# Kernel tuning notes

Hardware: AMD Instinct MI355X
Metric: run time of the kernel (lower is better)

The kernel has to match this reference:

```python
import jax, jax.numpy as jnp
import numpy as np

DIM = 512
NUM_HEADS = 8
HEAD_DIM = DIM // NUM_HEADS


def setup_inputs() -> dict:
    key = jax.random.key(0)
    ks = jax.random.split(key, 9)
    s = 1.0 / np.sqrt(DIM)
    x = jax.random.normal(ks[0], (2, 4096, DIM), dtype=jnp.float32)
    Wq = jax.random.uniform(ks[1], (DIM, DIM), jnp.float32, -s, s)
    bq = jax.random.uniform(ks[2], (DIM,), jnp.float32, -s, s)
    Wk = jax.random.uniform(ks[3], (DIM, DIM), jnp.float32, -s, s)
    bk = jax.random.uniform(ks[4], (DIM,), jnp.float32, -s, s)
    Wv = jax.random.uniform(ks[5], (DIM, DIM), jnp.float32, -s, s)
    bv = jax.random.uniform(ks[6], (DIM,), jnp.float32, -s, s)
    Wo = jax.random.uniform(ks[7], (DIM, DIM), jnp.float32, -s, s)
    bo = jax.random.uniform(ks[8], (DIM,), jnp.float32, -s, s)
    return {"x": x, "Wq": Wq, "bq": bq, "Wk": Wk, "bk": bk,
            "Wv": Wv, "bv": bv, "Wo": Wo, "bo": bo}


def reference(x, Wq, bq, Wk, bk, Wv, bv, Wo, bo):
    B, S, D = x.shape
    H, Hd = NUM_HEADS, HEAD_DIM
    # Linear layers (torch stores weight as [out,in]; here W is [in,out])
    q = (x @ Wq + bq).reshape(B, S, H, Hd).transpose(0, 2, 1, 3)  # [B,H,S,Hd]
    k = (x @ Wk + bk).reshape(B, S, H, Hd).transpose(0, 2, 1, 3)
    v = (x @ Wv + bv).reshape(B, S, H, Hd).transpose(0, 2, 1, 3)
    # NOTE: original scales by dim**0.5, not head_dim**0.5
    energy = jnp.einsum('bhqd,bhkd->bhqk', q, k) / jnp.sqrt(jnp.float32(D))
    attn = jax.nn.softmax(energy, axis=-1)
    out = jnp.einsum('bhqk,bhkd->bhqd', attn, v)
    out = out.transpose(0, 2, 1, 3).reshape(B, S, D)
    return out @ Wo + bo
```

## Files before the change

kernel.cpp:

```cpp
#include <hip/hip_runtime.h>

typedef unsigned short USH;
typedef short s16x8 __attribute__((ext_vector_type(8)));
typedef float f32x4 __attribute__((ext_vector_type(4)));
typedef float f32x4v __attribute__((ext_vector_type(4)));
typedef unsigned int u32x4 __attribute__((ext_vector_type(4)));
typedef s16x8 s16x8_a __attribute__((may_alias));
typedef f32x4v f32x4v_a __attribute__((may_alias));
typedef u32x4 u32x4_a __attribute__((may_alias));
typedef unsigned long long u64_a __attribute__((may_alias));

#if __has_builtin(__builtin_amdgcn_exp2f)
#define EXP2F(x) __builtin_amdgcn_exp2f(x)
#else
#define EXP2F(x) __builtin_exp2f(x)
#endif

__device__ __forceinline__ USH f2bf(float f) {
  union { float f; unsigned int i; } c; c.f = f;
  unsigned int x = c.i;
  return (USH)((x + 0x7FFFu + ((x >> 16) & 1u)) >> 16);
}
__device__ __forceinline__ unsigned int pk_bf16(float a, float b) {
  union { float f; unsigned int i; } ca, cb; ca.f = a; cb.f = b;
  return ((ca.i + 0x8000u) >> 16) | ((cb.i + 0x8000u) & 0xFFFF0000u);
}

__device__ __forceinline__ f32x4 mfma16(s16x8 a, s16x8 b, f32x4 c) {
  return __builtin_amdgcn_mfma_f32_16x16x32_bf16(a, b, c, 0, 0, 0);
}

__global__ void transpose_w(const float* __restrict__ Wq, const float* __restrict__ Wk,
                            const float* __restrict__ Wv, const float* __restrict__ Wo,
                            USH* __restrict__ wsT) {
  __shared__ float tile[32][33];
  const int z = blockIdx.z;
  const float* W = (z == 0) ? Wq : (z == 1) ? Wk : (z == 2) ? Wv : Wo;
  USH* WT = wsT + (size_t)z * 262144;
  const int n0 = blockIdx.x * 32, k0 = blockIdx.y * 32;
  const int tx = threadIdx.x, ty = threadIdx.y;
  #pragma unroll
  for (int i = 0; i < 4; ++i)
    tile[ty + i * 8][tx] = W[(size_t)(k0 + ty + i * 8) * 512 + n0 + tx];
  __syncthreads();
  #pragma unroll
  for (int i = 0; i < 4; ++i)
    WT[(size_t)(n0 + ty + i * 8) * 512 + k0 + tx] = f2bf(tile[tx][ty + i * 8]);
}

__global__ __launch_bounds__(256) void cvt_x(const float* __restrict__ x,
                                             USH* __restrict__ xb) {
  const size_t i = ((size_t)blockIdx.x * 256 + threadIdx.x) * 8;
  const f32x4v a = *(const f32x4v_a*)(x + i);
  const f32x4v b = *(const f32x4v_a*)(x + i + 4);
  u32x4 s;
  s.x = pk_bf16(a.x, a.y); s.y = pk_bf16(a.z, a.w);
  s.z = pk_bf16(b.x, b.y); s.w = pk_bf16(b.z, b.w);
  *(u32x4_a*)(xb + i) = s;
}

template <int MODE>
__global__ __launch_bounds__(256, 2) void gemm_bias(
    const USH* __restrict__ A, const USH* __restrict__ BT0,
    const float* __restrict__ b0, const float* __restrict__ b1,
    const float* __restrict__ b2,
    USH* __restrict__ oQ, USH* __restrict__ oKV, float* __restrict__ oF) {
  __shared__ __align__(16) USH As[128 * 36];
  __shared__ __align__(16) USH Bs[128 * 36];
  const int z = blockIdx.z;
  const USH* BT = BT0 + (size_t)z * 262144;
  const float* bias = (z == 0) ? b0 : ((z == 1) ? b1 : b2);
  USH* outb = (z == 0) ? oQ : (oKV + (size_t)(z - 1) * 4194304);
  const float qs = (MODE == 1 && z == 0) ? 0.06375871528132839f : 1.0f;

  const int t = threadIdx.x;
  const int w = t >> 6, lane = t & 63;
  const int c = lane & 15, g = lane >> 4;
  const int wm = w & 1, wn = w >> 1;
  const int m0 = blockIdx.x * 128, n0 = blockIdx.y * 128;
  const int srow = t >> 1, scol = (t & 1) * 16;

  f32x4 acc[4][4] = {};

  const USH* Ap0 = A + (size_t)(m0 + srow) * 512 + scol;
  const USH* Bp0 = BT + (size_t)(n0 + srow) * 512 + scol;
  s16x8 pa0 = *(const s16x8_a*)(Ap0);
  s16x8 pa1 = *(const s16x8_a*)(Ap0 + 8);
  s16x8 pb0 = *(const s16x8_a*)(Bp0);
  s16x8 pb1 = *(const s16x8_a*)(Bp0 + 8);

  for (int kt = 0; kt < 16; ++kt) {
    __syncthreads();
    *(s16x8_a*)(As + srow * 36 + scol) = pa0;
    *(s16x8_a*)(As + srow * 36 + scol + 8) = pa1;
    *(s16x8_a*)(Bs + srow * 36 + scol) = pb0;
    *(s16x8_a*)(Bs + srow * 36 + scol + 8) = pb1;
    const int ktn = (kt < 15) ? kt + 1 : kt;
    pa0 = *(const s16x8_a*)(Ap0 + ktn * 32);
    pa1 = *(const s16x8_a*)(Ap0 + ktn * 32 + 8);
    pb0 = *(const s16x8_a*)(Bp0 + ktn * 32);
    pb1 = *(const s16x8_a*)(Bp0 + ktn * 32 + 8);
    __syncthreads();
    s16x8 af[4], bfr[4];
    #pragma unroll
    for (int i = 0; i < 4; ++i) {
      af[i]  = *(const s16x8_a*)(As + (wm * 64 + i * 16 + c) * 36 + g * 8);
      bfr[i] = *(const s16x8_a*)(Bs + (wn * 64 + i * 16 + c) * 36 + g * 8);
    }
    #pragma unroll
    for (int mf = 0; mf < 4; ++mf)
      #pragma unroll
      for (int nf = 0; nf < 4; ++nf)
        acc[mf][nf] = mfma16(af[mf], bfr[nf], acc[mf][nf]);
  }

  #pragma unroll
  for (int nf = 0; nf < 4; ++nf) {
    const int n = n0 + wn * 64 + nf * 16 + c;
    const float bv = bias[n];
    #pragma unroll
    for (int mf = 0; mf < 4; ++mf)
      #pragma unroll
      for (int r = 0; r < 4; ++r) {
        const int m = m0 + wm * 64 + mf * 16 + g * 4 + r;
        const float v = (acc[mf][nf][r] + bv) * qs;
        if (MODE == 0) {
          oF[(size_t)m * 512 + n] = v;
        } else {
          const int bb = m >> 12, s = m & 4095, h = n >> 6, hd = n & 63;
          if (z == 2)
            outb[(((size_t)(bb * 8 + h)) * 64 + hd) * 4096 + s] = f2bf(v);
          else
            outb[(((size_t)(bb * 8 + h)) * 4096 + s) * 64 + hd] = f2bf(v);
        }
      }
  }
}

__global__ __launch_bounds__(256, 2) void attn(const USH* __restrict__ Qbuf,
                                               const USH* __restrict__ kv,
                                               USH* __restrict__ att) {
  __shared__ __align__(16) USH Ks[2 * 64 * 36];
  __shared__ __align__(16) USH Vt[64 * 76];
  __shared__ __align__(16) USH Ps[4][32 * 76];
  __shared__ float lbuf[4][32];

  const int t = threadIdx.x;
  const int w = t >> 6, lane = t & 63;
  const int c = lane & 15, g = lane >> 4;
  const int bh = blockIdx.y;
  const int bb = bh >> 3, hh = bh & 7;
  const size_t base = (size_t)bh * 262144;
  const USH* Q = Qbuf + base;
  const USH* K = kv + base;
  const USH* V = kv + 4194304 + base;
  const int q0 = blockIdx.x * 128 + w * 32;

  s16x8 qf[2][2];
  #pragma unroll
  for (int colf = 0; colf < 2; ++colf)
    #pragma unroll
    for (int kh = 0; kh < 2; ++kh)
      qf[colf][kh] = *(const s16x8_a*)(Q + (size_t)(q0 + colf * 16 + c) * 64 + kh * 32 + g * 8);

  s16x8 onesf;
  {
    const short one = (short)0x3F80, val = (c == 0) ? one : (short)0;
    #pragma unroll
    for (int j = 0; j < 8; ++j) onesf[j] = val;
  }

  f32x4 o[2][4] = {};
  f32x4 o_l[2] = {};
  const int kr = t >> 2, kc = (t & 3) * 16;
  const USH* Kp0 = K + (size_t)kr * 64 + kc;
  const USH* Vp0 = V + (size_t)kr * 4096 + kc;
  const int khalf = kc >> 5, koff = kc & 31;

  s16x8 pk0 = *(const s16x8_a*)(Kp0);
  s16x8 pk1 = *(const s16x8_a*)(Kp0 + 8);
  s16x8 pv0 = *(const s16x8_a*)(Vp0);
  s16x8 pv1 = *(const s16x8_a*)(Vp0 + 8);

  for (int kt = 0; kt < 64; ++kt) {
    __syncthreads();
    *(s16x8_a*)(Ks + khalf * 2304 + kr * 36 + koff) = pk0;
    *(s16x8_a*)(Ks + khalf * 2304 + kr * 36 + koff + 8) = pk1;
    *(s16x8_a*)(Vt + kr * 76 + kc) = pv0;
    *(s16x8_a*)(Vt + kr * 76 + kc + 8) = pv1;
    const int ktn = (kt < 63) ? kt + 1 : kt;
    pk0 = *(const s16x8_a*)(Kp0 + (size_t)ktn * 4096);
    pk1 = *(const s16x8_a*)(Kp0 + (size_t)ktn * 4096 + 8);
    pv0 = *(const s16x8_a*)(Vp0 + ktn * 64);
    pv1 = *(const s16x8_a*)(Vp0 + ktn * 64 + 8);
    __syncthreads();

    f32x4 st[4][2] = {};
    #pragma unroll
    for (int kh = 0; kh < 2; ++kh) {
      s16x8 ak[4];
      #pragma unroll
      for (int kff = 0; kff < 4; ++kff)
        ak[kff] = *(const s16x8_a*)(Ks + kh * 2304 + (kff * 16 + c) * 36 + g * 8);
      #pragma unroll
      for (int kff = 0; kff < 4; ++kff)
        #pragma unroll
        for (int colf = 0; colf < 2; ++colf)
          st[kff][colf] = mfma16(ak[kff], qf[colf][kh], st[kff][colf]);
    }

    #pragma unroll
    for (int colf = 0; colf < 2; ++colf)
      #pragma unroll
      for (int kff = 0; kff < 4; ++kff)
        #pragma unroll
        for (int r = 0; r < 4; ++r)
          st[kff][colf][r] = EXP2F(st[kff][colf][r]);

    #pragma unroll
    for (int colf = 0; colf < 2; ++colf)
      #pragma unroll
      for (int kff = 0; kff < 4; ++kff) {
        const unsigned int lo = pk_bf16(st[kff][colf][0], st[kff][colf][1]);
        const unsigned int hi = pk_bf16(st[kff][colf][2], st[kff][colf][3]);
        const unsigned long long pk64 =
            (unsigned long long)lo | ((unsigned long long)hi << 32);
        *(u64_a*)(&Ps[w][(c + 16 * colf) * 76 + kff * 16 + g * 4]) = pk64;
      }

    #pragma unroll
    for (int kf = 0; kf < 2; ++kf) {
      s16x8 ap[2], bv[4];
      #pragma unroll
      for (int mf = 0; mf < 2; ++mf)
        ap[mf] = *(const s16x8_a*)(&Ps[w][(mf * 16 + c) * 76 + kf * 32 + g * 8]);
      #pragma unroll
      for (int hf = 0; hf < 4; ++hf)
        bv[hf] = *(const s16x8_a*)(&Vt[(c + 16 * hf) * 76 + kf * 32 + g * 8]);
      #pragma unroll
      for (int mf = 0; mf < 2; ++mf) {
        #pragma unroll
        for (int hf = 0; hf < 4; ++hf)
          o[mf][hf] = mfma16(ap[mf], bv[hf], o[mf][hf]);
        o_l[mf] = mfma16(ap[mf], onesf, o_l[mf]);
      }
    }
  }

  if (c == 0) {
    #pragma unroll
    for (int mf = 0; mf < 2; ++mf)
      #pragma unroll
      for (int r = 0; r < 4; ++r)
        lbuf[w][mf * 16 + g * 4 + r] = o_l[mf][r];
  }
  __syncthreads();

  #pragma unroll
  for (int mf = 0; mf < 2; ++mf)
    #pragma unroll
    for (int r = 0; r < 4; ++r) {
      const int ml = mf * 16 + g * 4 + r;
      const float linv = 1.0f / lbuf[w][ml];
      const int qrow = q0 + ml;
      #pragma unroll
      for (int hf = 0; hf < 4; ++hf) {
        const int hd = c + 16 * hf;
        att[((size_t)(bb * 4096 + qrow)) * 512 + hh * 64 + hd] =
            f2bf(o[mf][hf][r] * linv);
      }
    }
}

extern "C" void kernel_launch(void* const* d_in, const int* in_sizes, int n_in,
                              void* d_out, int out_size, void* d_ws, size_t ws_size,
                              hipStream_t stream) {
  (void)in_sizes; (void)n_in; (void)out_size; (void)ws_size;
  const float* x  = (const float*)d_in[0];
  const float* Wq = (const float*)d_in[1];
  const float* bq = (const float*)d_in[2];
  const float* Wk = (const float*)d_in[3];
  const float* bk = (const float*)d_in[4];
  const float* Wv = (const float*)d_in[5];
  const float* bv = (const float*)d_in[6];
  const float* Wo = (const float*)d_in[7];
  const float* bo = (const float*)d_in[8];
  USH* ws  = (USH*)d_ws;
  USH* wT  = ws;
  USH* kv  = ws + 1048576;
  USH* att = ws + 1048576 + 8388608;
  float* outF = (float*)d_out;
  USH* qscratch = (USH*)d_out;
  USH* xb = (USH*)d_out + 4194304;

  transpose_w<<<dim3(16, 16, 4), dim3(32, 8), 0, stream>>>(Wq, Wk, Wv, Wo, wT);
  cvt_x<<<2048, 256, 0, stream>>>(x, xb);
  gemm_bias<1><<<dim3(64, 4, 3), 256, 0, stream>>>(xb, wT, bq, bk, bv,
                                                   qscratch, kv, nullptr);
  attn<<<dim3(32, 16), 256, 0, stream>>>(qscratch, kv, att);
  gemm_bias<0><<<dim3(64, 4, 1), 256, 0, stream>>>(att, wT + 3 * 262144, bo, bo, bo,
                                                   nullptr, nullptr, outF);
}
```

Before: 215.1 us.

## Double-buffer LDS tiles, fuse prep kernels, use hardware bf16 pack

Double-buffers the shared-memory K/V and GEMM tiles so each loop iteration needs only one barrier instead of two. Merges the weight transpose and x conversion into a single prep launch. Uses the native packed bf16 conversion builtin when the compiler provides it, and raises the GEMM occupancy hint to 3. This doubles LDS use for those tiles, and the rounding of the builtin may differ slightly from the manual rounding it replaces.

After: 225.1 us. 4.7% more time.

```diff
diff --git a/kernel.cpp b/kernel.cpp
--- a/kernel.cpp
+++ b/kernel.cpp
@@ -22,23 +22,46 @@
   return (USH)((x + 0x7FFFu + ((x >> 16) & 1u)) >> 16);
 }
 __device__ __forceinline__ unsigned int pk_bf16(float a, float b) {
+#if __has_builtin(__builtin_amdgcn_cvt_pk_bf16_f32)
+  typedef USH ush2 __attribute__((ext_vector_type(2)));
+  union { ush2 v; unsigned int u; } r;
+  r.v = __builtin_amdgcn_cvt_pk_bf16_f32(a, b);
+  return r.u;
+#else
   union { float f; unsigned int i; } ca, cb; ca.f = a; cb.f = b;
   return ((ca.i + 0x8000u) >> 16) | ((cb.i + 0x8000u) & 0xFFFF0000u);
+#endif
 }
 
 __device__ __forceinline__ f32x4 mfma16(s16x8 a, s16x8 b, f32x4 c) {
   return __builtin_amdgcn_mfma_f32_16x16x32_bf16(a, b, c, 0, 0, 0);
 }
 
-__global__ void transpose_w(const float* __restrict__ Wq, const float* __restrict__ Wk,
-                            const float* __restrict__ Wv, const float* __restrict__ Wo,
-                            USH* __restrict__ wsT) {
+__global__ __launch_bounds__(256) void prep(
+    const float* __restrict__ Wq, const float* __restrict__ Wk,
+    const float* __restrict__ Wv, const float* __restrict__ Wo,
+    const float* __restrict__ x, USH* __restrict__ wsT, USH* __restrict__ xb) {
   __shared__ float tile[32][33];
   const int z = blockIdx.z;
+  const int t = threadIdx.x;
+  if (z == 4) {
+    const size_t b0 = ((size_t)blockIdx.y * 16 + blockIdx.x) * 16384;
+    #pragma unroll
+    for (int j = 0; j < 8; ++j) {
+      const size_t i = b0 + (size_t)j * 2048 + t * 8;
+      const f32x4v a = *(const f32x4v_a*)(x + i);
+      const f32x4v b = *(const f32x4v_a*)(x + i + 4);
+      u32x4 s;
+      s.x = pk_bf16(a.x, a.y); s.y = pk_bf16(a.z, a.w);
+      s.z = pk_bf16(b.x, b.y); s.w = pk_bf16(b.z, b.w);
+      *(u32x4_a*)(xb + i) = s;
+    }
+    return;
+  }
   const float* W = (z == 0) ? Wq : (z == 1) ? Wk : (z == 2) ? Wv : Wo;
   USH* WT = wsT + (size_t)z * 262144;
   const int n0 = blockIdx.x * 32, k0 = blockIdx.y * 32;
-  const int tx = threadIdx.x, ty = threadIdx.y;
+  const int tx = t & 31, ty = t >> 5;
   #pragma unroll
   for (int i = 0; i < 4; ++i)
     tile[ty + i * 8][tx] = W[(size_t)(k0 + ty + i * 8) * 512 + n0 + tx];
@@ -48,25 +71,14 @@
     WT[(size_t)(n0 + ty + i * 8) * 512 + k0 + tx] = f2bf(tile[tx][ty + i * 8]);
 }
 
-__global__ __launch_bounds__(256) void cvt_x(const float* __restrict__ x,
-                                             USH* __restrict__ xb) {
-  const size_t i = ((size_t)blockIdx.x * 256 + threadIdx.x) * 8;
-  const f32x4v a = *(const f32x4v_a*)(x + i);
-  const f32x4v b = *(const f32x4v_a*)(x + i + 4);
-  u32x4 s;
-  s.x = pk_bf16(a.x, a.y); s.y = pk_bf16(a.z, a.w);
-  s.z = pk_bf16(b.x, b.y); s.w = pk_bf16(b.z, b.w);
-  *(u32x4_a*)(xb + i) = s;
-}
-
 template <int MODE>
-__global__ __launch_bounds__(256, 2) void gemm_bias(
+__global__ __launch_bounds__(256, 3) void gemm_bias(
     const USH* __restrict__ A, const USH* __restrict__ BT0,
     const float* __restrict__ b0, const float* __restrict__ b1,
     const float* __restrict__ b2,
     USH* __restrict__ oQ, USH* __restrict__ oKV, float* __restrict__ oF) {
-  __shared__ __align__(16) USH As[128 * 36];
-  __shared__ __align__(16) USH Bs[128 * 36];
+  __shared__ __align__(16) USH As[2][128 * 36];
+  __shared__ __align__(16) USH Bs[2][128 * 36];
   const int z = blockIdx.z;
   const USH* BT = BT0 + (size_t)z * 262144;
   const float* bias = (z == 0) ? b0 : ((z == 1) ? b1 : b2);
@@ -90,22 +102,22 @@
   s16x8 pb1 = *(const s16x8_a*)(Bp0 + 8);
 
   for (int kt = 0; kt < 16; ++kt) {
+    const int buf = kt & 1;
+    *(s16x8_a*)(As[buf] + srow * 36 + scol) = pa0;
+    *(s16x8_a*)(As[buf] + srow * 36 + scol + 8) = pa1;
+    *(s16x8_a*)(Bs[buf] + srow * 36 + scol) = pb0;
+    *(s16x8_a*)(Bs[buf] + srow * 36 + scol + 8) = pb1;
     __syncthreads();
-    *(s16x8_a*)(As + srow * 36 + scol) = pa0;
-    *(s16x8_a*)(As + srow * 36 + scol + 8) = pa1;
-    *(s16x8_a*)(Bs + srow * 36 + scol) = pb0;
-    *(s16x8_a*)(Bs + srow * 36 + scol + 8) = pb1;
     const int ktn = (kt < 15) ? kt + 1 : kt;
     pa0 = *(const s16x8_a*)(Ap0 + ktn * 32);
     pa1 = *(const s16x8_a*)(Ap0 + ktn * 32 + 8);
     pb0 = *(const s16x8_a*)(Bp0 + ktn * 32);
     pb1 = *(const s16x8_a*)(Bp0 + ktn * 32 + 8);
-    __syncthreads();
     s16x8 af[4], bfr[4];
     #pragma unroll
     for (int i = 0; i < 4; ++i) {
-      af[i]  = *(const s16x8_a*)(As + (wm * 64 + i * 16 + c) * 36 + g * 8);
-      bfr[i] = *(const s16x8_a*)(Bs + (wn * 64 + i * 16 + c) * 36 + g * 8);
+      af[i]  = *(const s16x8_a*)(As[buf] + (wm * 64 + i * 16 + c) * 36 + g * 8);
+      bfr[i] = *(const s16x8_a*)(Bs[buf] + (wn * 64 + i * 16 + c) * 36 + g * 8);
     }
     #pragma unroll
     for (int mf = 0; mf < 4; ++mf)
@@ -140,8 +152,8 @@
 __global__ __launch_bounds__(256, 2) void attn(const USH* __restrict__ Qbuf,
                                                const USH* __restrict__ kv,
                                                USH* __restrict__ att) {
-  __shared__ __align__(16) USH Ks[2 * 64 * 36];
-  __shared__ __align__(16) USH Vt[64 * 76];
+  __shared__ __align__(16) USH Ks[2][2 * 64 * 36];
+  __shared__ __align__(16) USH Vt[2][64 * 76];
   __shared__ __align__(16) USH Ps[4][32 * 76];
   __shared__ float lbuf[4][32];
 
@@ -183,17 +195,17 @@
   s16x8 pv1 = *(const s16x8_a*)(Vp0 + 8);
 
   for (int kt = 0; kt < 64; ++kt) {
+    const int buf = kt & 1;
+    *(s16x8_a*)(Ks[buf] + khalf * 2304 + kr * 36 + koff) = pk0;
+    *(s16x8_a*)(Ks[buf] + khalf * 2304 + kr * 36 + koff + 8) = pk1;
+    *(s16x8_a*)(Vt[buf] + kr * 76 + kc) = pv0;
+    *(s16x8_a*)(Vt[buf] + kr * 76 + kc + 8) = pv1;
     __syncthreads();
-    *(s16x8_a*)(Ks + khalf * 2304 + kr * 36 + koff) = pk0;
-    *(s16x8_a*)(Ks + khalf * 2304 + kr * 36 + koff + 8) = pk1;
-    *(s16x8_a*)(Vt + kr * 76 + kc) = pv0;
-    *(s16x8_a*)(Vt + kr * 76 + kc + 8) = pv1;
     const int ktn = (kt < 63) ? kt + 1 : kt;
     pk0 = *(const s16x8_a*)(Kp0 + (size_t)ktn * 4096);
     pk1 = *(const s16x8_a*)(Kp0 + (size_t)ktn * 4096 + 8);
     pv0 = *(const s16x8_a*)(Vp0 + ktn * 64);
     pv1 = *(const s16x8_a*)(Vp0 + ktn * 64 + 8);
-    __syncthreads();
 
     f32x4 st[4][2] = {};
     #pragma unroll
@@ -201,7 +213,7 @@
       s16x8 ak[4];
       #pragma unroll
       for (int kff = 0; kff < 4; ++kff)
-        ak[kff] = *(const s16x8_a*)(Ks + kh * 2304 + (kff * 16 + c) * 36 + g * 8);
+        ak[kff] = *(const s16x8_a*)(Ks[buf] + kh * 2304 + (kff * 16 + c) * 36 + g * 8);
       #pragma unroll
       for (int kff = 0; kff < 4; ++kff)
         #pragma unroll
@@ -236,7 +248,7 @@
         ap[mf] = *(const s16x8_a*)(&Ps[w][(mf * 16 + c) * 76 + kf * 32 + g * 8]);
       #pragma unroll
       for (int hf = 0; hf < 4; ++hf)
-        bv[hf] = *(const s16x8_a*)(&Vt[(c + 16 * hf) * 76 + kf * 32 + g * 8]);
+        bv[hf] = *(const s16x8_a*)(Vt[buf] + (c + 16 * hf) * 76 + kf * 32 + g * 8);
       #pragma unroll
       for (int mf = 0; mf < 2; ++mf) {
         #pragma unroll
@@ -293,8 +305,7 @@
   USH* qscratch = (USH*)d_out;
   USH* xb = (USH*)d_out + 4194304;
 
-  transpose_w<<<dim3(16, 16, 4), dim3(32, 8), 0, stream>>>(Wq, Wk, Wv, Wo, wT);
-  cvt_x<<<2048, 256, 0, stream>>>(x, xb);
+  prep<<<dim3(16, 16, 5), 256, 0, stream>>>(Wq, Wk, Wv, Wo, x, wT, xb);
   gemm_bias<1><<<dim3(64, 4, 3), 256, 0, stream>>>(xb, wT, bq, bk, bv,
                                                    qscratch, kv, nullptr);
   attn<<<dim3(32, 16), 256, 0, stream>>>(qscratch, kv, att);
```

## Load K/V fragments directly from global memory, drop LDS staging and barriers

Applied to the files above, without the earlier changes.

The attention kernel no longer stages K and V tiles through shared memory with two __syncthreads per iteration. Each wave now loads its MFMA operand fragments for K and transposed V straight from global memory, relying on L1/L2 to serve the repeated reads across the four waves. The bf16 pack helper also uses the hardware cvt_pk_bf16_f32 builtin when it is available. This trades barrier and LDS traffic for more global and cache load traffic and higher load latency in the inner loop, which has no software prefetch.

After: 348.4 us. 1.62x slower.

```diff
diff --git a/kernel.cpp b/kernel.cpp
--- a/kernel.cpp
+++ b/kernel.cpp
@@ -22,8 +22,15 @@
   return (USH)((x + 0x7FFFu + ((x >> 16) & 1u)) >> 16);
 }
 __device__ __forceinline__ unsigned int pk_bf16(float a, float b) {
+#if __has_builtin(__builtin_amdgcn_cvt_pk_bf16_f32)
+  typedef USH ush2 __attribute__((ext_vector_type(2)));
+  union { ush2 v; unsigned int u; } r;
+  r.v = __builtin_amdgcn_cvt_pk_bf16_f32(a, b);
+  return r.u;
+#else
   union { float f; unsigned int i; } ca, cb; ca.f = a; cb.f = b;
   return ((ca.i + 0x8000u) >> 16) | ((cb.i + 0x8000u) & 0xFFFF0000u);
+#endif
 }
 
 __device__ __forceinline__ f32x4 mfma16(s16x8 a, s16x8 b, f32x4 c) {
@@ -140,8 +147,6 @@
 __global__ __launch_bounds__(256, 2) void attn(const USH* __restrict__ Qbuf,
                                                const USH* __restrict__ kv,
                                                USH* __restrict__ att) {
-  __shared__ __align__(16) USH Ks[2 * 64 * 36];
-  __shared__ __align__(16) USH Vt[64 * 76];
   __shared__ __align__(16) USH Ps[4][32 * 76];
   __shared__ float lbuf[4][32];
 
@@ -172,36 +177,17 @@
 
   f32x4 o[2][4] = {};
   f32x4 o_l[2] = {};
-  const int kr = t >> 2, kc = (t & 3) * 16;
-  const USH* Kp0 = K + (size_t)kr * 64 + kc;
-  const USH* Vp0 = V + (size_t)kr * 4096 + kc;
-  const int khalf = kc >> 5, koff = kc & 31;
-
-  s16x8 pk0 = *(const s16x8_a*)(Kp0);
-  s16x8 pk1 = *(const s16x8_a*)(Kp0 + 8);
-  s16x8 pv0 = *(const s16x8_a*)(Vp0);
-  s16x8 pv1 = *(const s16x8_a*)(Vp0 + 8);
+  const USH* Kp = K + (size_t)c * 64 + g * 8;
+  const USH* Vp = V + (size_t)c * 4096 + g * 8;
 
   for (int kt = 0; kt < 64; ++kt) {
-    __syncthreads();
-    *(s16x8_a*)(Ks + khalf * 2304 + kr * 36 + koff) = pk0;
-    *(s16x8_a*)(Ks + khalf * 2304 + kr * 36 + koff + 8) = pk1;
-    *(s16x8_a*)(Vt + kr * 76 + kc) = pv0;
-    *(s16x8_a*)(Vt + kr * 76 + kc + 8) = pv1;
-    const int ktn = (kt < 63) ? kt + 1 : kt;
-    pk0 = *(const s16x8_a*)(Kp0 + (size_t)ktn * 4096);
-    pk1 = *(const s16x8_a*)(Kp0 + (size_t)ktn * 4096 + 8);
-    pv0 = *(const s16x8_a*)(Vp0 + ktn * 64);
-    pv1 = *(const s16x8_a*)(Vp0 + ktn * 64 + 8);
-    __syncthreads();
-
     f32x4 st[4][2] = {};
     #pragma unroll
     for (int kh = 0; kh < 2; ++kh) {
       s16x8 ak[4];
       #pragma unroll
       for (int kff = 0; kff < 4; ++kff)
-        ak[kff] = *(const s16x8_a*)(Ks + kh * 2304 + (kff * 16 + c) * 36 + g * 8);
+        ak[kff] = *(const s16x8_a*)(Kp + (size_t)(kt * 64 + kff * 16) * 64 + kh * 32);
       #pragma unroll
       for (int kff = 0; kff < 4; ++kff)
         #pragma unroll
@@ -236,7 +222,7 @@
         ap[mf] = *(const s16x8_a*)(&Ps[w][(mf * 16 + c) * 76 + kf * 32 + g * 8]);
       #pragma unroll
       for (int hf = 0; hf < 4; ++hf)
-        bv[hf] = *(const s16x8_a*)(&Vt[(c + 16 * hf) * 76 + kf * 32 + g * 8]);
+        bv[hf] = *(const s16x8_a*)(Vp + (size_t)hf * 16 * 4096 + kt * 64 + kf * 32);
       #pragma unroll
       for (int mf = 0; mf < 2; ++mf) {
         #pragma unroll
```
